# Kernel optimization log

Measured on AMD Instinct MI355X. Metric: run time of the kernel, lower is better.

Reference implementation:

```python
import jax, jax.numpy as jnp
import numpy as np


def setup_inputs() -> dict:
    key = jax.random.key(0)
    k1, k2, k3, k4, k5 = jax.random.split(key, 5)
    B, C, H, W = 2, 3, 64, 64
    f_tar = jax.random.normal(k1, (B, C, H, W), dtype=jnp.float32)
    f_src = jax.random.normal(k2, (B, C, H, W), dtype=jnp.float32)
    # Pinhole intrinsics (focal=50, principal point at image center) + small noise,
    # guaranteed invertible.
    K_base = jnp.array([[50.0, 0.0, 32.0], [0.0, 50.0, 32.0], [0.0, 0.0, 1.0]],
                       dtype=jnp.float32)
    K = K_base[None] + 0.05 * jax.random.normal(k3, (B, 3, 3), dtype=jnp.float32)
    # Near-identity rotation-like matrix.
    R = jnp.eye(3, dtype=jnp.float32)[None] + 0.1 * jax.random.normal(
        k4, (B, 3, 3), dtype=jnp.float32)
    t = jax.random.normal(k5, (B, 3, 1), dtype=jnp.float32)
    return {"f_tar": f_tar, "f_src": f_src, "K": K, "R": R, "t": t}


def reference(f_tar, f_src, K, R, t):
    B, C, H, W = f_src.shape  # C == 3 (required by the cross product)
    N = H * W
    dtype = f_src.dtype

    f_src_flat = f_src.reshape(B, C, N)  # (B, 3, N)
    f_tar_flat = f_tar.reshape(B, C, N)  # (B, 3, N)

    # A[b, i, j] = <f_src[:, i], f_tar[:, j]>  -> (B, N, N)
    A = jnp.einsum('bci,bcj->bij', f_src_flat, f_tar_flat)

    # Homogeneous pixel coordinates (3, N): rows of meshgrid(H, W, indexing='ij').
    ix, iy = jnp.meshgrid(jnp.arange(H), jnp.arange(W), indexing='ij')
    pix = jnp.stack([ix.reshape(-1), iy.reshape(-1), jnp.ones(N, dtype=jnp.int32)],
                    axis=0).astype(dtype)  # (3, N)

    K_inv = jnp.linalg.inv(K)  # (B, 3, 3)
    # tar_proj = K @ (R @ (K^-1 @ x) + t)   -> (B, 3, N)
    cam_rays = jnp.einsum('bij,jn->bin', K_inv, pix)
    tar_proj = jnp.einsum('bij,bjn->bin', K, jnp.einsum('bij,bjn->bin', R, cam_rays) + t)
    # Origin projects to K @ (R @ 0 + t) = K @ t, broadcast over N.
    o_proj = jnp.einsum('bij,bjn->bin', K, t)  # (B, 3, 1)

    diff = tar_proj - o_proj  # (B, 3, N)

    # Epipolar distance: || (f_src - o) x diff || / ||diff||, broadcast to (B, N, N).
    a = f_src_flat[:, :, :, None] - o_proj[:, :, :, None]  # (B, 3, N, 1)
    b = diff[:, :, None, :]                                 # (B, 3, 1, N)
    cross = jnp.cross(a, b, axis=1)                         # (B, 3, N, N)
    cross_norm = jnp.linalg.norm(cross, axis=1)             # (B, N, N)
    diff_norm = jnp.linalg.norm(diff, axis=1, keepdims=True)  # (B, 1, N)
    d_epipolar = cross_norm / diff_norm                     # (B, N, N)

    # 'sigmoid' in the original is nn.Softmax(dim=-1).
    EPI_THRESH = 0.5
    SHARPNESS = 50.0
    weight_map = 1.0 - jax.nn.softmax(SHARPNESS * (d_epipolar - EPI_THRESH), axis=-1)

    A_weighted = A * weight_map
    attention_map = jax.nn.softmax(A_weighted, axis=1)  # normalize over src positions

    # (B, N, N) @ (B, N, C) -> (B, N, C), then raw view back to (B, C, H, W)
    attended = jnp.einsum('bik,bck->bic', attention_map, f_src_flat)
    return attended.reshape(B, C, H, W)
```

## Files before the change

kernel.cpp:

```cpp
#include <hip/hip_runtime.h>

namespace {
constexpr int BB = 2;
constexpr int NN = 4096;
constexpr float LOG2E = 1.44269504088896340736f;
constexpr float T50 = 72.1347520444481703f;
constexpr float T50SQ = T50 * T50;

constexpr int OFF_W4   = 0;
constexpr int OFF_IREC = 4 * BB * NN;
constexpr int OFF_JREC = 12 * BB * NN;
constexpr int OFF_NMAX = 24 * BB * NN;
}

__device__ __forceinline__ float fsqrt(float x) { return __builtin_amdgcn_sqrtf(x); }
__device__ __forceinline__ float fexp2(float x) {
#if __has_builtin(__builtin_amdgcn_exp2f)
  return __builtin_amdgcn_exp2f(x);
#else
  return exp2f(x);
#endif
}
__device__ __forceinline__ float flog2(float x) {
#if __has_builtin(__builtin_amdgcn_logf)
  return __builtin_amdgcn_logf(x);
#else
  return log2f(x);
#endif
}

__global__ __launch_bounds__(256) void k_setup(
    const float* __restrict__ fsrc, const float* __restrict__ ftar,
    const float* __restrict__ Kb, const float* __restrict__ Rb,
    const float* __restrict__ tb, float* __restrict__ ws) {
  int gid = blockIdx.x * 256 + threadIdx.x;
  if (gid >= BB * NN) return;
  int b = gid >> 12;
  int n = gid & (NN - 1);

  float K[9], R[9], t3[3];
#pragma unroll
  for (int k = 0; k < 9; k++) { K[k] = Kb[b * 9 + k]; R[k] = Rb[b * 9 + k]; }
#pragma unroll
  for (int k = 0; k < 3; k++) t3[k] = tb[b * 3 + k];

  float c00 = K[4] * K[8] - K[5] * K[7];
  float c01 = K[5] * K[6] - K[3] * K[8];
  float c02 = K[3] * K[7] - K[4] * K[6];
  float det = K[0] * c00 + K[1] * c01 + K[2] * c02;
  float id = 1.0f / det;
  float Ki[9];
  Ki[0] = c00 * id; Ki[1] = (K[2] * K[7] - K[1] * K[8]) * id; Ki[2] = (K[1] * K[5] - K[2] * K[4]) * id;
  Ki[3] = c01 * id; Ki[4] = (K[0] * K[8] - K[2] * K[6]) * id; Ki[5] = (K[2] * K[3] - K[0] * K[5]) * id;
  Ki[6] = c02 * id; Ki[7] = (K[1] * K[6] - K[0] * K[7]) * id; Ki[8] = (K[0] * K[4] - K[1] * K[3]) * id;

  float RK[9];
#pragma unroll
  for (int i = 0; i < 3; i++)
#pragma unroll
    for (int j = 0; j < 3; j++)
      RK[i * 3 + j] = R[i * 3 + 0] * Ki[j] + R[i * 3 + 1] * Ki[3 + j] + R[i * 3 + 2] * Ki[6 + j];
  float M3[9];
#pragma unroll
  for (int i = 0; i < 3; i++)
#pragma unroll
    for (int j = 0; j < 3; j++)
      M3[i * 3 + j] = K[i * 3 + 0] * RK[j] + K[i * 3 + 1] * RK[3 + j] + K[i * 3 + 2] * RK[6 + j];
  float o0 = K[0] * t3[0] + K[1] * t3[1] + K[2] * t3[2];
  float o1 = K[3] * t3[0] + K[4] * t3[1] + K[5] * t3[2];
  float o2 = K[6] * t3[0] + K[7] * t3[1] + K[8] * t3[2];

  float sx = fsrc[b * 3 * NN + 0 * NN + n];
  float sy = fsrc[b * 3 * NN + 1 * NN + n];
  float sz = fsrc[b * 3 * NN + 2 * NN + n];
  float tx = ftar[b * 3 * NN + 0 * NN + n];
  float ty = ftar[b * 3 * NN + 1 * NN + n];
  float tz = ftar[b * 3 * NN + 2 * NN + n];

  float ux = sx - o0, uy = sy - o1, uz = sz - o2;
  float usq = ux * ux + uy * uy + uz * uz;

  float px = (float)(n >> 6), py = (float)(n & 63);
  float vx = M3[0] * px + M3[1] * py + M3[2];
  float vy = M3[3] * px + M3[4] * py + M3[5];
  float vz = M3[6] * px + M3[7] * py + M3[8];
  float invn = rsqrtf(vx * vx + vy * vy + vz * vz) * T50;
  float wx = vx * invn, wy = vy * invn, wz = vz * invn;
  float tn = fsqrt(tx * tx + ty * ty + tz * tz);

  float4* w4 = (float4*)(ws + OFF_W4);
  float4* irec = (float4*)(ws + OFF_IREC);
  float4* jrec = (float4*)(ws + OFF_JREC);
  w4[gid] = make_float4(wx, wy, wz, 0.f);
  irec[gid * 2 + 0] = make_float4(ux, uy, uz, usq * T50SQ);
  irec[gid * 2 + 1] = make_float4(sx * LOG2E, sy * LOG2E, sz * LOG2E, 0.f);
  jrec[gid * 3 + 0] = make_float4(wx, wy, wz, tn);
  jrec[gid * 3 + 1] = make_float4(tx, ty, tz, 0.f);
  jrec[gid * 3 + 2] = make_float4(sx, sy, sz, 0.f);

  float ns = fsqrt(sx * sx + sy * sy + sz * sz);
#pragma unroll
  for (int off = 32; off; off >>= 1) ns = fmaxf(ns, __shfl_xor(ns, off));
  if ((threadIdx.x & 63) == 0)
    atomicMax((unsigned int*)(ws + OFF_NMAX + b), __float_as_uint(ns));
}

__global__ __launch_bounds__(256, 4) void k_p1(float* __restrict__ ws) {
  __shared__ float sred[4][8];
  __shared__ float smax[8];
  const float4* irec = (const float4*)(ws + OFF_IREC);
  int tid = threadIdx.x, wid = tid >> 6, lane = tid & 63;
  int g0 = blockIdx.x * 8;
  int b = g0 >> 12;
  const float4* wb = (const float4*)(ws + OFF_W4) + b * NN;

  float ux[8], uy[8], uz[8], us[8];
#pragma unroll
  for (int r = 0; r < 8; r++) {
    float4 u = irec[(g0 + r) * 2];
    ux[r] = u.x; uy[r] = u.y; uz[r] = u.z; us[r] = u.w;
  }

  float mx[8] = {0.f, 0.f, 0.f, 0.f, 0.f, 0.f, 0.f, 0.f};
  for (int j = wid * 64 + lane; j < NN; j += 512) {
    float4 w0 = wb[j];
    float4 w1 = wb[j + 256];
#pragma unroll
    for (int r = 0; r < 8; r++) {
      float d0 = ux[r] * w0.x + uy[r] * w0.y + uz[r] * w0.z;
      float d1 = ux[r] * w1.x + uy[r] * w1.y + uz[r] * w1.z;
      mx[r] = fmaxf(mx[r], fmaxf(__builtin_fmaf(-d0, d0, us[r]),
                                 __builtin_fmaf(-d1, d1, us[r])));
    }
  }
#pragma unroll
  for (int off = 32; off; off >>= 1)
#pragma unroll
    for (int r = 0; r < 8; r++) mx[r] = fmaxf(mx[r], __shfl_xor(mx[r], off));
  if (lane == 0) {
#pragma unroll
    for (int r = 0; r < 8; r++) sred[wid][r] = mx[r];
  }
  __syncthreads();
  if (tid < 8)
    smax[tid] = fsqrt(fmaxf(fmaxf(fmaxf(sred[0][tid], sred[1][tid]),
                                  fmaxf(sred[2][tid], sred[3][tid])), 0.f));
  __syncthreads();
  float m[8];
#pragma unroll
  for (int r = 0; r < 8; r++) m[r] = smax[r];

  float s[8] = {0.f, 0.f, 0.f, 0.f, 0.f, 0.f, 0.f, 0.f};
  for (int j = wid * 64 + lane; j < NN; j += 512) {
    float4 w0 = wb[j];
    float4 w1 = wb[j + 256];
#pragma unroll
    for (int r = 0; r < 8; r++) {
      float d0 = ux[r] * w0.x + uy[r] * w0.y + uz[r] * w0.z;
      float d1 = ux[r] * w1.x + uy[r] * w1.y + uz[r] * w1.z;
      float q0 = fmaxf(__builtin_fmaf(-d0, d0, us[r]), 0.f);
      float q1 = fmaxf(__builtin_fmaf(-d1, d1, us[r]), 0.f);
      s[r] += fexp2(fsqrt(q0) - m[r]) + fexp2(fsqrt(q1) - m[r]);
    }
  }
#pragma unroll
  for (int off = 32; off; off >>= 1)
#pragma unroll
    for (int r = 0; r < 8; r++) s[r] += __shfl_xor(s[r], off);
  if (lane == 0) {
#pragma unroll
    for (int r = 0; r < 8; r++) sred[wid][r] = s[r];
  }
  __syncthreads();
  if (tid < 8) {
    float tot = sred[0][tid] + sred[1][tid] + sred[2][tid] + sred[3][tid];
    ws[OFF_IREC + (g0 + tid) * 8 + 7] = smax[tid] + flog2(tot);
  }
}

__global__ __launch_bounds__(256, 4) void k_p2(float* __restrict__ ws) {
  __shared__ float sred[4][8];
  const float4* irec = (const float4*)(ws + OFF_IREC);
  const float4* jrec = (const float4*)(ws + OFF_JREC);
  int tid = threadIdx.x, wid = tid >> 6, lane = tid & 63;
  int c0 = (blockIdx.x >> 1) * 8;
  int half = blockIdx.x & 1;
  int b = c0 >> 12;
  int base = b * NN;
  float maxns2 = ws[OFF_NMAX + b] * LOG2E;

  float wx[8], wy[8], wz[8], tx[8], ty[8], tz[8], Mb2[8];
#pragma unroll
  for (int r = 0; r < 8; r++) {
    float4 q0 = jrec[(c0 + r) * 3 + 0];
    float4 q1 = jrec[(c0 + r) * 3 + 1];
    wx[r] = q0.x; wy[r] = q0.y; wz[r] = q0.z;
    Mb2[r] = maxns2 * q0.w;
    tx[r] = q1.x; ty[r] = q1.y; tz[r] = q1.z;
  }

  float S[8] = {0.f, 0.f, 0.f, 0.f, 0.f, 0.f, 0.f, 0.f};
  int i0 = half * (NN / 2);
  for (int i = i0 + wid * 64 + lane; i < i0 + NN / 2; i += 256) {
    int idx = base + i;
    float4 u = irec[idx * 2 + 0];
    float4 sq = irec[idx * 2 + 1];
#pragma unroll
    for (int r = 0; r < 8; r++) {
      float dot = u.x * wx[r] + u.y * wy[r] + u.z * wz[r];
      float d2 = fmaxf(__builtin_fmaf(-dot, dot, u.w), 0.f);
      float en = fexp2(fsqrt(d2) - sq.w);
      float wgt = 1.f - en;
      float A2 = sq.x * tx[r] + sq.y * ty[r] + sq.z * tz[r];
      S[r] += fexp2(__builtin_fmaf(A2, wgt, -Mb2[r]));
    }
  }
#pragma unroll
  for (int off = 32; off; off >>= 1)
#pragma unroll
    for (int r = 0; r < 8; r++) S[r] += __shfl_xor(S[r], off);
  if (lane == 0) {
#pragma unroll
    for (int r = 0; r < 8; r++) sred[wid][r] = S[r];
  }
  __syncthreads();
  if (tid < 8) {
    float tot = sred[0][tid] + sred[1][tid] + sred[2][tid] + sred[3][tid];
    atomicAdd(ws + OFF_JREC + (c0 + tid) * 12 + 7, tot);
  }
}

__global__ __launch_bounds__(256, 4) void k_p3(const float* __restrict__ ws,
                                               float* __restrict__ out) {
  __shared__ float sacc[4][24];
  const float4* irec = (const float4*)(ws + OFF_IREC);
  const float4* jrec = (const float4*)(ws + OFF_JREC);
  int tid = threadIdx.x, wid = tid >> 6, lane = tid & 63;
  int g0 = (blockIdx.x >> 1) * 8;
  int half = blockIdx.x & 1;
  int b = g0 >> 12;
  int base = b * NN;
  float maxns2 = ws[OFF_NMAX + b] * LOG2E;

  float ux[8], uy[8], uz[8], us[8], ml[8], s2x[8], s2y[8], s2z[8];
#pragma unroll
  for (int r = 0; r < 8; r++) {
    float4 u = irec[(g0 + r) * 2 + 0];
    float4 sq = irec[(g0 + r) * 2 + 1];
    ux[r] = u.x; uy[r] = u.y; uz[r] = u.z; us[r] = u.w;
    s2x[r] = sq.x; s2y[r] = sq.y; s2z[r] = sq.z; ml[r] = sq.w;
  }
  float acc[8][3];
#pragma unroll
  for (int r = 0; r < 8; r++) { acc[r][0] = 0.f; acc[r][1] = 0.f; acc[r][2] = 0.f; }

  int j0 = half * (NN / 2);
  for (int j = j0 + wid * 64 + lane; j < j0 + NN / 2; j += 256) {
    int idx = base + j;
    float4 q0 = jrec[idx * 3 + 0];
    float4 q1 = jrec[idx * 3 + 1];
    float4 q2 = jrec[idx * 3 + 2];
    float cst = __builtin_fmaf(maxns2, q0.w, flog2(q1.w));
#pragma unroll
    for (int r = 0; r < 8; r++) {
      float dot = ux[r] * q0.x + uy[r] * q0.y + uz[r] * q0.z;
      float d2 = fmaxf(__builtin_fmaf(-dot, dot, us[r]), 0.f);
      float en = fexp2(fsqrt(d2) - ml[r]);
      float wgt = 1.f - en;
      float A2 = s2x[r] * q1.x + s2y[r] * q1.y + s2z[r] * q1.z;
      float p = fexp2(__builtin_fmaf(A2, wgt, -cst));
      acc[r][0] = __builtin_fmaf(p, q2.x, acc[r][0]);
      acc[r][1] = __builtin_fmaf(p, q2.y, acc[r][1]);
      acc[r][2] = __builtin_fmaf(p, q2.z, acc[r][2]);
    }
  }
#pragma unroll
  for (int off = 32; off; off >>= 1)
#pragma unroll
    for (int r = 0; r < 8; r++) {
      acc[r][0] += __shfl_xor(acc[r][0], off);
      acc[r][1] += __shfl_xor(acc[r][1], off);
      acc[r][2] += __shfl_xor(acc[r][2], off);
    }
  if (lane == 0) {
#pragma unroll
    for (int r = 0; r < 8; r++) {
      sacc[wid][r * 3 + 0] = acc[r][0];
      sacc[wid][r * 3 + 1] = acc[r][1];
      sacc[wid][r * 3 + 2] = acc[r][2];
    }
  }
  __syncthreads();
  if (tid < 24) {
    float v = sacc[0][tid] + sacc[1][tid] + sacc[2][tid] + sacc[3][tid];
    atomicAdd(out + g0 * 3 + tid, v);
  }
}

extern "C" void kernel_launch(void* const* d_in, const int* in_sizes, int n_in,
                              void* d_out, int out_size, void* d_ws, size_t ws_size,
                              hipStream_t stream) {
  (void)in_sizes; (void)n_in; (void)ws_size;
  const float* ftar = (const float*)d_in[0];
  const float* fsrc = (const float*)d_in[1];
  const float* K = (const float*)d_in[2];
  const float* R = (const float*)d_in[3];
  const float* t = (const float*)d_in[4];
  float* ws = (float*)d_ws;
  float* out = (float*)d_out;

  hipMemsetAsync((char*)d_ws + OFF_NMAX * sizeof(float), 0, BB * sizeof(float), stream);
  hipMemsetAsync(d_out, 0, out_size, stream);

  k_setup<<<dim3(32), dim3(256), 0, stream>>>(fsrc, ftar, K, R, t, ws);
  k_p1<<<dim3(1024), dim3(256), 0, stream>>>(ws);
  k_p2<<<dim3(2048), dim3(256), 0, stream>>>(ws);
  k_p3<<<dim3(2048), dim3(256), 0, stream>>>(ws, out);
}
```

Before: 130.2 us.

## Restructure p2/p3 to one column per thread with chunked inner loop and atomics

Rewrites the column-sum and output-accumulation kernels so each thread owns one column (p2) or one row (p3) and loops over a 128-element chunk of the other dimension. Every lane in a wavefront reads the same record at the same time, so those loads become broadcasts. The change also removes the wavefront shuffle reductions and shared-memory reductions, replacing them with per-thread atomics across 32 chunks. In exchange it gives up the 8-row register reuse of the old kernels and raises the number of global atomics.

New measurement: 169.0 us. +29.8%, slower.

```diff
diff --git a/kernel.cpp b/kernel.cpp
--- a/kernel.cpp
+++ b/kernel.cpp
@@ -6,6 +6,8 @@
 constexpr float LOG2E = 1.44269504088896340736f;
 constexpr float T50 = 72.1347520444481703f;
 constexpr float T50SQ = T50 * T50;
+constexpr int ICH = 32;
+constexpr int JCH = 32;
 
 constexpr int OFF_W4   = 0;
 constexpr int OFF_IREC = 4 * BB * NN;
@@ -178,123 +180,77 @@
   }
 }
 
-__global__ __launch_bounds__(256, 4) void k_p2(float* __restrict__ ws) {
-  __shared__ float sred[4][8];
+__global__ __launch_bounds__(256) void k_p2t(float* __restrict__ ws) {
+  int tid = threadIdx.x;
+  int g = blockIdx.x / ICH;
+  int ic = blockIdx.x % ICH;
+  int col = g * 256 + tid;
+  int b = col >> 12;
+  int base = b * NN;
   const float4* irec = (const float4*)(ws + OFF_IREC);
   const float4* jrec = (const float4*)(ws + OFF_JREC);
-  int tid = threadIdx.x, wid = tid >> 6, lane = tid & 63;
-  int c0 = (blockIdx.x >> 1) * 8;
-  int half = blockIdx.x & 1;
-  int b = c0 >> 12;
-  int base = b * NN;
   float maxns2 = ws[OFF_NMAX + b] * LOG2E;
 
-  float wx[8], wy[8], wz[8], tx[8], ty[8], tz[8], Mb2[8];
-#pragma unroll
-  for (int r = 0; r < 8; r++) {
-    float4 q0 = jrec[(c0 + r) * 3 + 0];
-    float4 q1 = jrec[(c0 + r) * 3 + 1];
-    wx[r] = q0.x; wy[r] = q0.y; wz[r] = q0.z;
-    Mb2[r] = maxns2 * q0.w;
-    tx[r] = q1.x; ty[r] = q1.y; tz[r] = q1.z;
-  }
-
-  float S[8] = {0.f, 0.f, 0.f, 0.f, 0.f, 0.f, 0.f, 0.f};
-  int i0 = half * (NN / 2);
-  for (int i = i0 + wid * 64 + lane; i < i0 + NN / 2; i += 256) {
-    int idx = base + i;
+  float4 q0 = jrec[col * 3 + 0];
+  float4 q1 = jrec[col * 3 + 1];
+  float wx = q0.x, wy = q0.y, wz = q0.z;
+  float Mb2 = maxns2 * q0.w;
+  float tx = q1.x, ty = q1.y, tz = q1.z;
+
+  float S = 0.f;
+  int i0 = base + ic * (NN / ICH);
+#pragma unroll 4
+  for (int it = 0; it < NN / ICH; ++it) {
+    int idx = i0 + it;
     float4 u = irec[idx * 2 + 0];
     float4 sq = irec[idx * 2 + 1];
-#pragma unroll
-    for (int r = 0; r < 8; r++) {
-      float dot = u.x * wx[r] + u.y * wy[r] + u.z * wz[r];
-      float d2 = fmaxf(__builtin_fmaf(-dot, dot, u.w), 0.f);
-      float en = fexp2(fsqrt(d2) - sq.w);
-      float wgt = 1.f - en;
-      float A2 = sq.x * tx[r] + sq.y * ty[r] + sq.z * tz[r];
-      S[r] += fexp2(__builtin_fmaf(A2, wgt, -Mb2[r]));
-    }
-  }
-#pragma unroll
-  for (int off = 32; off; off >>= 1)
-#pragma unroll
-    for (int r = 0; r < 8; r++) S[r] += __shfl_xor(S[r], off);
-  if (lane == 0) {
-#pragma unroll
-    for (int r = 0; r < 8; r++) sred[wid][r] = S[r];
-  }
-  __syncthreads();
-  if (tid < 8) {
-    float tot = sred[0][tid] + sred[1][tid] + sred[2][tid] + sred[3][tid];
-    atomicAdd(ws + OFF_JREC + (c0 + tid) * 12 + 7, tot);
-  }
-}
-
-__global__ __launch_bounds__(256, 4) void k_p3(const float* __restrict__ ws,
-                                               float* __restrict__ out) {
-  __shared__ float sacc[4][24];
+    float dot = u.x * wx + u.y * wy + u.z * wz;
+    float d2 = fmaxf(__builtin_fmaf(-dot, dot, u.w), 0.f);
+    float en = fexp2(fsqrt(d2) - sq.w);
+    float wgt = 1.f - en;
+    float A2 = sq.x * tx + sq.y * ty + sq.z * tz;
+    S += fexp2(__builtin_fmaf(A2, wgt, -Mb2));
+  }
+  atomicAdd(ws + OFF_JREC + col * 12 + 7, S);
+}
+
+__global__ __launch_bounds__(256) void k_p3t(const float* __restrict__ ws,
+                                             float* __restrict__ out) {
+  int tid = threadIdx.x;
+  int g = blockIdx.x / JCH;
+  int jc = blockIdx.x % JCH;
+  int row = g * 256 + tid;
+  int b = row >> 12;
+  int base = b * NN;
   const float4* irec = (const float4*)(ws + OFF_IREC);
   const float4* jrec = (const float4*)(ws + OFF_JREC);
-  int tid = threadIdx.x, wid = tid >> 6, lane = tid & 63;
-  int g0 = (blockIdx.x >> 1) * 8;
-  int half = blockIdx.x & 1;
-  int b = g0 >> 12;
-  int base = b * NN;
   float maxns2 = ws[OFF_NMAX + b] * LOG2E;
 
-  float ux[8], uy[8], uz[8], us[8], ml[8], s2x[8], s2y[8], s2z[8];
-#pragma unroll
-  for (int r = 0; r < 8; r++) {
-    float4 u = irec[(g0 + r) * 2 + 0];
-    float4 sq = irec[(g0 + r) * 2 + 1];
-    ux[r] = u.x; uy[r] = u.y; uz[r] = u.z; us[r] = u.w;
-    s2x[r] = sq.x; s2y[r] = sq.y; s2z[r] = sq.z; ml[r] = sq.w;
-  }
-  float acc[8][3];
-#pragma unroll
-  for (int r = 0; r < 8; r++) { acc[r][0] = 0.f; acc[r][1] = 0.f; acc[r][2] = 0.f; }
-
-  int j0 = half * (NN / 2);
-  for (int j = j0 + wid * 64 + lane; j < j0 + NN / 2; j += 256) {
-    int idx = base + j;
+  float4 u = irec[row * 2 + 0];
+  float4 sq = irec[row * 2 + 1];
+  float a0 = 0.f, a1 = 0.f, a2 = 0.f;
+
+  int j0 = base + jc * (NN / JCH);
+#pragma unroll 2
+  for (int it = 0; it < NN / JCH; ++it) {
+    int idx = j0 + it;
     float4 q0 = jrec[idx * 3 + 0];
     float4 q1 = jrec[idx * 3 + 1];
     float4 q2 = jrec[idx * 3 + 2];
     float cst = __builtin_fmaf(maxns2, q0.w, flog2(q1.w));
-#pragma unroll
-    for (int r = 0; r < 8; r++) {
-      float dot = ux[r] * q0.x + uy[r] * q0.y + uz[r] * q0.z;
-      float d2 = fmaxf(__builtin_fmaf(-dot, dot, us[r]), 0.f);
-      float en = fexp2(fsqrt(d2) - ml[r]);
-      float wgt = 1.f - en;
-      float A2 = s2x[r] * q1.x + s2y[r] * q1.y + s2z[r] * q1.z;
-      float p = fexp2(__builtin_fmaf(A2, wgt, -cst));
-      acc[r][0] = __builtin_fmaf(p, q2.x, acc[r][0]);
-      acc[r][1] = __builtin_fmaf(p, q2.y, acc[r][1]);
-      acc[r][2] = __builtin_fmaf(p, q2.z, acc[r][2]);
-    }
-  }
-#pragma unroll
-  for (int off = 32; off; off >>= 1)
-#pragma unroll
-    for (int r = 0; r < 8; r++) {
-      acc[r][0] += __shfl_xor(acc[r][0], off);
-      acc[r][1] += __shfl_xor(acc[r][1], off);
-      acc[r][2] += __shfl_xor(acc[r][2], off);
-    }
-  if (lane == 0) {
-#pragma unroll
-    for (int r = 0; r < 8; r++) {
-      sacc[wid][r * 3 + 0] = acc[r][0];
-      sacc[wid][r * 3 + 1] = acc[r][1];
-      sacc[wid][r * 3 + 2] = acc[r][2];
-    }
-  }
-  __syncthreads();
-  if (tid < 24) {
-    float v = sacc[0][tid] + sacc[1][tid] + sacc[2][tid] + sacc[3][tid];
-    atomicAdd(out + g0 * 3 + tid, v);
-  }
+    float dot = u.x * q0.x + u.y * q0.y + u.z * q0.z;
+    float d2 = fmaxf(__builtin_fmaf(-dot, dot, u.w), 0.f);
+    float en = fexp2(fsqrt(d2) - sq.w);
+    float wgt = 1.f - en;
+    float A2 = sq.x * q1.x + sq.y * q1.y + sq.z * q1.z;
+    float p = fexp2(__builtin_fmaf(A2, wgt, -cst));
+    a0 = __builtin_fmaf(p, q2.x, a0);
+    a1 = __builtin_fmaf(p, q2.y, a1);
+    a2 = __builtin_fmaf(p, q2.z, a2);
+  }
+  atomicAdd(out + row * 3 + 0, a0);
+  atomicAdd(out + row * 3 + 1, a1);
+  atomicAdd(out + row * 3 + 2, a2);
 }
 
 extern "C" void kernel_launch(void* const* d_in, const int* in_sizes, int n_in,
@@ -314,6 +270,6 @@
 
   k_setup<<<dim3(32), dim3(256), 0, stream>>>(fsrc, ftar, K, R, t, ws);
   k_p1<<<dim3(1024), dim3(256), 0, stream>>>(ws);
-  k_p2<<<dim3(2048), dim3(256), 0, stream>>>(ws);
-  k_p3<<<dim3(2048), dim3(256), 0, stream>>>(ws, out);
-}
+  k_p2t<<<dim3(32 * ICH), dim3(256), 0, stream>>>(ws);
+  k_p3t<<<dim3(32 * JCH), dim3(256), 0, stream>>>(ws, out);
+}
```
